# Optimization experiments

Measured on AMD Instinct MI355X. Metric: run time of the kernel, lower is better.

## Reference

```python
import jax, jax.numpy as jnp
import numpy as np

B, N, E, H = 16, 1024, 1024, 16
D = E // H  # head size = 64

def setup_inputs() -> dict:
    key = jax.random.key(0)
    ks = jax.random.split(key, 5)
    s = 1.0 / np.sqrt(E)
    return {
        "x": jax.random.normal(ks[0], (B, N, E), dtype=jnp.float32),
        "W_qkv": jax.random.normal(ks[1], (E, 3 * E), dtype=jnp.float32) * s,
        "b_qkv": jnp.zeros((3 * E,), dtype=jnp.float32),
        "W_proj": jax.random.normal(ks[2], (E, E), dtype=jnp.float32) * s,
        "b_proj": jnp.zeros((E,), dtype=jnp.float32),
    }

def reference(x, W_qkv, b_qkv, W_proj, b_proj):
    # qkv projection: [B,N,3E]
    qkv = x @ W_qkv + b_qkv
    q, k, v = jnp.split(qkv, 3, axis=-1)
    # b n (h d) -> b h n d
    def split_heads(t):
        return t.reshape(B, N, H, D).transpose(0, 2, 1, 3)
    q, k, v = split_heads(q), split_heads(k), split_heads(v)
    scale = D ** -0.5
    attn = jnp.einsum('bhnd,bhmd->bhnm', q, k) * scale  # [B,H,N,N]
    attn = jax.nn.softmax(attn, axis=-1)
    # dropout p=0 -> identity
    o = jnp.einsum('bhnm,bhmd->bhnd', attn, v)  # [B,H,N,D]
    o = o.transpose(0, 2, 1, 3).reshape(B, N, E)  # b h n d -> b n (h d)
    return o @ W_proj + b_proj
```

## Files before the change

kernel.cpp:

```cpp
#include <hip/hip_runtime.h>
#include <hip/hip_bf16.h>
#include <math.h>

#define BB 16
#define NN 1024
#define EE 1024
#define HH 16
#define DD 64
#define THREE_E 3072
#define M_TOTAL (BB * NN)

typedef __attribute__((ext_vector_type(8))) short bf16x8;
typedef __attribute__((ext_vector_type(4))) short bf16x4;
typedef __attribute__((ext_vector_type(4))) float floatx4;

#define SCALE_Q 0.18033688011112042f

static __device__ __forceinline__ unsigned short f2bf(float f) {
    union { float f; unsigned u; } x; x.f = f;
    unsigned r = x.u + 0x7fffu + ((x.u >> 16) & 1u);
    return (unsigned short)(r >> 16);
}

static __device__ __forceinline__ bf16x8 pack8v(floatx4 a, floatx4 b) {
    union { bf16x8 v; unsigned u[4]; } r;
    __hip_bfloat162 t;
    t = __float22bfloat162_rn(make_float2(a[0], a[1])); r.u[0] = *(unsigned*)&t;
    t = __float22bfloat162_rn(make_float2(a[2], a[3])); r.u[1] = *(unsigned*)&t;
    t = __float22bfloat162_rn(make_float2(b[0], b[1])); r.u[2] = *(unsigned*)&t;
    t = __float22bfloat162_rn(make_float2(b[2], b[3])); r.u[3] = *(unsigned*)&t;
    return r.v;
}
static __device__ __forceinline__ bf16x8 pack8f(float4 a, float4 b) {
    union { bf16x8 v; unsigned u[4]; } r;
    __hip_bfloat162 t;
    t = __float22bfloat162_rn(make_float2(a.x, a.y)); r.u[0] = *(unsigned*)&t;
    t = __float22bfloat162_rn(make_float2(a.z, a.w)); r.u[1] = *(unsigned*)&t;
    t = __float22bfloat162_rn(make_float2(b.x, b.y)); r.u[2] = *(unsigned*)&t;
    t = __float22bfloat162_rn(make_float2(b.z, b.w)); r.u[3] = *(unsigned*)&t;
    return r.v;
}

#define ASYNC16(gp, lp)                                                \
    __builtin_amdgcn_global_load_lds(                                  \
        (const __attribute__((address_space(1))) void*)(gp),           \
        (__attribute__((address_space(3))) void*)(lp), 16, 0, 0)

#define DRAIN_VMEM() __asm__ __volatile__("s_waitcnt vmcnt(0)" ::: "memory")

__global__ __launch_bounds__(256) void convert_x(
    const float* __restrict__ x, unsigned short* __restrict__ xb)
{
    int i = blockIdx.x * 256 + threadIdx.x;
    const float4* xp = (const float4*)x;
    float4 a = xp[i * 2], b = xp[i * 2 + 1];
    *(bf16x8*)&xb[i * 8] = pack8f(a, b);
}

__global__ __launch_bounds__(256) void wtrans(
    const float* __restrict__ w, unsigned short* __restrict__ wt, int R, int C)
{
    __shared__ float tile[32][33];
    const int t = threadIdx.x;
    const int lr = t >> 5, lc = t & 31;
    const int r0 = blockIdx.y * 32, c0 = blockIdx.x * 32;
    #pragma unroll
    for (int p = 0; p < 4; ++p)
        tile[lr + p * 8][lc] = w[(size_t)(r0 + lr + p * 8) * C + c0 + lc];
    __syncthreads();
    #pragma unroll
    for (int p = 0; p < 4; ++p) {
        int oc = lr + p * 8;
        float v = tile[lc][oc];
        wt[(size_t)(c0 + oc) * R + r0 + lc] = f2bf(v);
    }
}

__global__ __launch_bounds__(256) void gemm_qkv_mfma(
    const unsigned short* __restrict__ xb,
    const unsigned short* __restrict__ wt,
    const float* __restrict__ bias,
    unsigned short* __restrict__ Qo, unsigned short* __restrict__ Ko,
    unsigned short* __restrict__ Vo)
{
    __shared__ __align__(16) unsigned short As[128 * 32];
    __shared__ __align__(16) unsigned short Bs[128 * 32];

    const int t = threadIdx.x;
    const int w = t >> 6, lane = t & 63;
    const int quad = lane >> 4, l15 = lane & 15;
    const int wm = w >> 1, wn = w & 1;
    const int m0 = blockIdx.y * 128;
    const int n0 = blockIdx.x * 128;
    const int srow = lane >> 2;
    const int scw = (((lane & 3) ^ ((srow ^ (srow >> 2)) & 3))) * 8;
    const int rsw = ((quad ^ ((l15 ^ (l15 >> 2)) & 3))) * 8;

    floatx4 acc[4][4];
    #pragma unroll
    for (int i = 0; i < 4; ++i)
        #pragma unroll
        for (int j = 0; j < 4; ++j) acc[i][j] = (floatx4){0.f, 0.f, 0.f, 0.f};

    for (int kk = 0; kk < EE; kk += 32) {
        #pragma unroll
        for (int r = 0; r < 2; ++r) {
            int c = w * 2 + r;
            ASYNC16(&xb[(size_t)(m0 + c * 16 + srow) * EE + kk + scw],
                    &As[c * 512]);
            ASYNC16(&wt[(size_t)(n0 + c * 16 + srow) * EE + kk + scw],
                    &Bs[c * 512]);
        }
        DRAIN_VMEM();
        __syncthreads();

        bf16x8 af[4], bf[4];
        #pragma unroll
        for (int i = 0; i < 4; ++i) {
            af[i] = *(const bf16x8*)&As[(wm * 64 + i * 16 + l15) * 32 + rsw];
            bf[i] = *(const bf16x8*)&Bs[(wn * 64 + i * 16 + l15) * 32 + rsw];
        }
        #pragma unroll
        for (int i = 0; i < 4; ++i)
            #pragma unroll
            for (int j = 0; j < 4; ++j)
                acc[i][j] = __builtin_amdgcn_mfma_f32_16x16x32_bf16(
                    af[i], bf[j], acc[i][j], 0, 0, 0);
        __syncthreads();
    }

    const int mb = m0 + wm * 64;
    const int nb = n0 + wn * 64;
    #pragma unroll
    for (int i = 0; i < 4; ++i) {
        #pragma unroll
        for (int j = 0; j < 4; ++j) {
            int nc = nb + j * 16;
            int which = nc >> 10;
            int e0 = nc & 1023;
            int h  = e0 >> 6;
            int d0 = e0 & 63;
            float bv = bias[nc + l15];
            #pragma unroll
            for (int r = 0; r < 4; ++r) {
                int m = mb + i * 16 + quad * 4 + r;
                int b = m >> 10, n = m & 1023;
                size_t off = ((size_t)(b * HH + h) * NN + n) * DD + d0 + l15;
                float v = acc[i][j][r] + bv;
                if (which == 0)      Qo[off] = f2bf(v * SCALE_Q);
                else if (which == 1) Ko[off] = f2bf(v);
                else                 Vo[off] = f2bf(v);
            }
        }
    }
}

__global__ __launch_bounds__(256) void vtrans(
    const unsigned short* __restrict__ V, unsigned short* __restrict__ Vt)
{
    __shared__ __align__(16) unsigned short tile[64][72];
    const int t  = threadIdx.x;
    const int bh = blockIdx.x;
    const int n0 = blockIdx.y * 64;
    const int r  = t >> 2, c = t & 3;

    const unsigned short* src = &V[((size_t)bh * NN + n0 + r) * DD + c * 16];
    bf16x8 v0 = *(const bf16x8*)&src[0];
    bf16x8 v1 = *(const bf16x8*)&src[8];
    #pragma unroll
    for (int k = 0; k < 8; ++k) tile[c * 16 + k][r]     = v0[k];
    #pragma unroll
    for (int k = 0; k < 8; ++k) tile[c * 16 + 8 + k][r] = v1[k];
    __syncthreads();

    unsigned short* dst = &Vt[((size_t)bh * DD + r) * NN + n0 + c * 16];
    *(bf16x8*)&dst[0] = *(const bf16x8*)&tile[r][c * 16];
    *(bf16x8*)&dst[8] = *(const bf16x8*)&tile[r][c * 16 + 8];
}

__global__ __launch_bounds__(256) void attn_mfma(
    const unsigned short* __restrict__ Q,
    const unsigned short* __restrict__ K,
    const unsigned short* __restrict__ Vt,
    unsigned short* __restrict__ O)
{
    __shared__ __align__(16) unsigned short Ks[64 * 64];
    __shared__ __align__(16) unsigned short Vs[64 * 64];

    const int t    = threadIdx.x;
    const int w    = t >> 6;
    const int quad = (t >> 4) & 3;
    const int l15  = t & 15;
    const int i    = blockIdx.x;
    const int bh   = ((i >> 6) << 3) | (i & 7);
    const int qt   = (i >> 3) & 7;

    const unsigned short* Qg = Q  + (size_t)bh * NN * DD;
    const unsigned short* Kg = K  + (size_t)bh * NN * DD;
    const unsigned short* Vg = Vt + (size_t)bh * DD * NN;

    const int q0 = qt * 128 + w * 32;

    bf16x8 qf[2][2];
    #pragma unroll
    for (int a = 0; a < 2; ++a) {
        qf[a][0] = *(const bf16x8*)&Qg[(size_t)(q0 + a * 16 + l15) * DD + quad * 8];
        qf[a][1] = *(const bf16x8*)&Qg[(size_t)(q0 + a * 16 + l15) * DD + 32 + quad * 8];
    }

    floatx4 oa[2][4];
    #pragma unroll
    for (int a = 0; a < 2; ++a)
        #pragma unroll
        for (int jd = 0; jd < 4; ++jd) oa[a][jd] = (floatx4){0.f, 0.f, 0.f, 0.f};
    float lsum[2] = {0.f, 0.f};

    const int srow = t >> 2;
    const int sc   = t & 3;
    const int swz  = srow & 7;
    const int cbase = ((quad ^ (l15 & 7)) << 3);

    bf16x8 kr0, kr1, vr0, vr1;
    {
        const unsigned short* kg = &Kg[(size_t)srow * DD + sc * 16];
        kr0 = *(const bf16x8*)&kg[0];
        kr1 = *(const bf16x8*)&kg[8];
        const unsigned short* vg = &Vg[(size_t)srow * NN + sc * 16];
        vr0 = *(const bf16x8*)&vg[0];
        vr1 = *(const bf16x8*)&vg[8];
    }

    for (int kt = 0; kt < 16; ++kt) {
        __syncthreads();
        *(bf16x8*)&Ks[srow * 64 + (((2 * sc + 0) ^ swz) << 3)] = kr0;
        *(bf16x8*)&Ks[srow * 64 + (((2 * sc + 1) ^ swz) << 3)] = kr1;
        {
            bf16x4 h[4];
            h[0] = (bf16x4){vr0[0], vr0[1], vr0[2], vr0[3]};
            h[1] = (bf16x4){vr0[4], vr0[5], vr0[6], vr0[7]};
            h[2] = (bf16x4){vr1[0], vr1[1], vr1[2], vr1[3]};
            h[3] = (bf16x4){vr1[4], vr1[5], vr1[6], vr1[7]};
            #pragma unroll
            for (int q = 0; q < 4; ++q) {
                int col = ((((sc >> 1) * 4 + q) ^ swz) << 3) + ((sc & 1) << 2);
                *(bf16x4*)&Vs[srow * 64 + col] = h[q];
            }
        }
        __syncthreads();

        if (kt < 15) {
            const unsigned short* kg =
                &Kg[(size_t)((kt + 1) * 64 + srow) * DD + sc * 16];
            kr0 = *(const bf16x8*)&kg[0];
            kr1 = *(const bf16x8*)&kg[8];
            const unsigned short* vg =
                &Vg[(size_t)srow * NN + (kt + 1) * 64 + sc * 16];
            vr0 = *(const bf16x8*)&vg[0];
            vr1 = *(const bf16x8*)&vg[8];
        }

        floatx4 sa[2][4];
        #pragma unroll
        for (int a = 0; a < 2; ++a)
            #pragma unroll
            for (int tt = 0; tt < 4; ++tt) sa[a][tt] = (floatx4){0.f, 0.f, 0.f, 0.f};
        #pragma unroll
        for (int tt = 0; tt < 4; ++tt) {
            const unsigned short* kb = &Ks[(tt * 16 + l15) * 64];
            bf16x8 kf0 = *(const bf16x8*)&kb[cbase];
            bf16x8 kf1 = *(const bf16x8*)&kb[cbase ^ 32];
            #pragma unroll
            for (int a = 0; a < 2; ++a) {
                sa[a][tt] = __builtin_amdgcn_mfma_f32_16x16x32_bf16(
                    kf0, qf[a][0], sa[a][tt], 0, 0, 0);
                sa[a][tt] = __builtin_amdgcn_mfma_f32_16x16x32_bf16(
                    kf1, qf[a][1], sa[a][tt], 0, 0, 0);
            }
        }

        bf16x8 pf[2][2];
        #pragma unroll
        for (int a = 0; a < 2; ++a) {
            floatx4 pe[4];
            #pragma unroll
            for (int tt = 0; tt < 4; ++tt) {
                #pragma unroll
                for (int r = 0; r < 4; ++r) {
                    float p = exp2f(sa[a][tt][r]);
                    pe[tt][r] = p;
                    lsum[a] += p;
                }
            }
            pf[a][0] = pack8v(pe[0], pe[1]);
            pf[a][1] = pack8v(pe[2], pe[3]);
        }

        #pragma unroll
        for (int jd = 0; jd < 4; ++jd) {
            const unsigned short* vb = &Vs[(jd * 16 + l15) * 64];
            bf16x8 vf0 = *(const bf16x8*)&vb[cbase];
            bf16x8 vf1 = *(const bf16x8*)&vb[cbase ^ 32];
            #pragma unroll
            for (int a = 0; a < 2; ++a) {
                oa[a][jd] = __builtin_amdgcn_mfma_f32_16x16x32_bf16(
                    vf0, pf[a][0], oa[a][jd], 0, 0, 0);
                oa[a][jd] = __builtin_amdgcn_mfma_f32_16x16x32_bf16(
                    vf1, pf[a][1], oa[a][jd], 0, 0, 0);
            }
        }
    }

    #pragma unroll
    for (int a = 0; a < 2; ++a) {
        lsum[a] += __shfl_xor(lsum[a], 16, 64);
        lsum[a] += __shfl_xor(lsum[a], 32, 64);
    }

    const int b = bh >> 4, h = bh & 15;
    #pragma unroll
    for (int a = 0; a < 2; ++a) {
        float inv = 1.f / lsum[a];
        int n = q0 + a * 16 + l15;
        size_t base = (size_t)(b * NN + n) * EE + h * DD;
        #pragma unroll
        for (int jd = 0; jd < 4; ++jd) {
            bf16x4 v;
            v[0] = (short)f2bf(oa[a][jd][0] * inv);
            v[1] = (short)f2bf(oa[a][jd][1] * inv);
            v[2] = (short)f2bf(oa[a][jd][2] * inv);
            v[3] = (short)f2bf(oa[a][jd][3] * inv);
            *(bf16x4*)&O[base + jd * 16 + quad * 4] = v;
        }
    }
}

__global__ __launch_bounds__(256) void gemm_proj_mfma(
    const unsigned short* __restrict__ Ob,
    const unsigned short* __restrict__ Bp,
    const float* __restrict__ bias, float* __restrict__ out)
{
    __shared__ __align__(16) unsigned short As[128 * 32];
    __shared__ __align__(16) unsigned short Bs[128 * 32];

    const int t = threadIdx.x;
    const int w = t >> 6, lane = t & 63;
    const int quad = lane >> 4, l15 = lane & 15;
    const int wm = w >> 1, wn = w & 1;
    const int m0 = blockIdx.y * 128;
    const int n0 = blockIdx.x * 128;
    const int srow = lane >> 2;
    const int scw = (((lane & 3) ^ ((srow ^ (srow >> 2)) & 3))) * 8;
    const int rsw = ((quad ^ ((l15 ^ (l15 >> 2)) & 3))) * 8;

    floatx4 acc[4][4];
    #pragma unroll
    for (int i = 0; i < 4; ++i)
        #pragma unroll
        for (int j = 0; j < 4; ++j) acc[i][j] = (floatx4){0.f, 0.f, 0.f, 0.f};

    for (int kk = 0; kk < EE; kk += 32) {
        #pragma unroll
        for (int r = 0; r < 2; ++r) {
            int c = w * 2 + r;
            ASYNC16(&Ob[(size_t)(m0 + c * 16 + srow) * EE + kk + scw],
                    &As[c * 512]);
            ASYNC16(&Bp[(size_t)(n0 + c * 16 + srow) * EE + kk + scw],
                    &Bs[c * 512]);
        }
        DRAIN_VMEM();
        __syncthreads();

        bf16x8 af[4], bf[4];
        #pragma unroll
        for (int i = 0; i < 4; ++i) {
            af[i] = *(const bf16x8*)&As[(wm * 64 + i * 16 + l15) * 32 + rsw];
            bf[i] = *(const bf16x8*)&Bs[(wn * 64 + i * 16 + l15) * 32 + rsw];
        }
        #pragma unroll
        for (int i = 0; i < 4; ++i)
            #pragma unroll
            for (int j = 0; j < 4; ++j)
                acc[i][j] = __builtin_amdgcn_mfma_f32_16x16x32_bf16(
                    af[i], bf[j], acc[i][j], 0, 0, 0);
        __syncthreads();
    }

    const int mb = m0 + wm * 64;
    const int nb = n0 + wn * 64;
    #pragma unroll
    for (int i = 0; i < 4; ++i) {
        #pragma unroll
        for (int j = 0; j < 4; ++j) {
            float bv = bias[nb + j * 16 + l15];
            #pragma unroll
            for (int r = 0; r < 4; ++r) {
                int mrow = mb + i * 16 + quad * 4 + r;
                out[(size_t)mrow * EE + nb + j * 16 + l15] = acc[i][j][r] + bv;
            }
        }
    }
}

extern "C" void kernel_launch(void* const* d_in, const int* in_sizes, int n_in,
                              void* d_out, int out_size, void* d_ws, size_t ws_size,
                              hipStream_t stream) {
    const float* x     = (const float*)d_in[0];
    const float* Wqkv  = (const float*)d_in[1];
    const float* bqkv  = (const float*)d_in[2];
    const float* Wproj = (const float*)d_in[3];
    const float* bproj = (const float*)d_in[4];
    float* out = (float*)d_out;

    const size_t BHND = (size_t)BB * HH * NN * DD;
    unsigned short* Q   = (unsigned short*)d_ws;
    unsigned short* K   = Q   + BHND;
    unsigned short* Vn  = K   + BHND;
    unsigned short* Vt  = Vn  + BHND;
    unsigned short* Ob  = Vt  + BHND;
    unsigned short* xb  = Ob  + BHND;
    unsigned short* Wqt = xb  + BHND;
    unsigned short* Wpt = Wqt + (size_t)THREE_E * EE;

    dim3 blk(256);
    convert_x<<<dim3(M_TOTAL * EE / (256 * 8)), blk, 0, stream>>>(x, xb);
    wtrans<<<dim3(THREE_E / 32, EE / 32), blk, 0, stream>>>(Wqkv, Wqt, EE, THREE_E);
    wtrans<<<dim3(EE / 32, EE / 32), blk, 0, stream>>>(Wproj, Wpt, EE, EE);

    gemm_qkv_mfma<<<dim3(THREE_E / 128, M_TOTAL / 128), blk, 0, stream>>>(
        xb, Wqt, bqkv, Q, K, Vn);
    vtrans<<<dim3(BB * HH, NN / 64), blk, 0, stream>>>(Vn, Vt);
    attn_mfma<<<dim3(BB * HH * NN / 128), blk, 0, stream>>>(Q, K, Vt, Ob);
    gemm_proj_mfma<<<dim3(EE / 128, M_TOTAL / 128), blk, 0, stream>>>(
        Ob, Wpt, bproj, out);
}
```

Before: 447.2 us.

## Pipeline QKV and projection GEMMs with 256x256 tiles and 4-stage async LDS

Both GEMMs move from 128x128 tiles with 256 threads and a full vmem drain every k-step to 256x256 tiles with 512 threads and a 4-slot LDS ring. Global-to-LDS loads are issued three steps ahead and split between the two MFMA halves, with partial vmcnt waits, raw barriers and s_setprio around the MFMA blocks. The block index is remapped across 8 groups, likely to spread tiles over XCDs for better cache locality. The change targets exposed load latency and low arithmetic intensity, at the cost of more registers (8x4 accumulators) and 128KB of LDS per block, which may limit occupancy.

```diff
diff --git a/kernel.cpp b/kernel.cpp
--- a/kernel.cpp
+++ b/kernel.cpp
@@ -46,8 +46,6 @@
         (const __attribute__((address_space(1))) void*)(gp),           \
         (__attribute__((address_space(3))) void*)(lp), 16, 0, 0)
 
-#define DRAIN_VMEM() __asm__ __volatile__("s_waitcnt vmcnt(0)" ::: "memory")
-
 __global__ __launch_bounds__(256) void convert_x(
     const float* __restrict__ x, unsigned short* __restrict__ xb)
 {
@@ -76,66 +74,107 @@
     }
 }
 
-__global__ __launch_bounds__(256) void gemm_qkv_mfma(
+#define GNT 32
+
+__global__ __launch_bounds__(512, 2) void gemm_qkv_mfma(
     const unsigned short* __restrict__ xb,
     const unsigned short* __restrict__ wt,
     const float* __restrict__ bias,
     unsigned short* __restrict__ Qo, unsigned short* __restrict__ Ko,
     unsigned short* __restrict__ Vo)
 {
-    __shared__ __align__(16) unsigned short As[128 * 32];
-    __shared__ __align__(16) unsigned short Bs[128 * 32];
+    __shared__ __align__(16) unsigned short As[4][256 * 32];
+    __shared__ __align__(16) unsigned short Bs[4][256 * 32];
 
     const int t = threadIdx.x;
     const int w = t >> 6, lane = t & 63;
     const int quad = lane >> 4, l15 = lane & 15;
-    const int wm = w >> 1, wn = w & 1;
-    const int m0 = blockIdx.y * 128;
-    const int n0 = blockIdx.x * 128;
+    const int wm = w >> 2, wn = w & 3;
+
+    const int id  = blockIdx.x;
+    const int sid = (id & 7) * ((int)gridDim.x >> 3) + (id >> 3);
+    const int m0 = (sid / 12) * 256;
+    const int n0 = (sid % 12) * 256;
+
     const int srow = lane >> 2;
     const int scw = (((lane & 3) ^ ((srow ^ (srow >> 2)) & 3))) * 8;
     const int rsw = ((quad ^ ((l15 ^ (l15 >> 2)) & 3))) * 8;
 
-    floatx4 acc[4][4];
-    #pragma unroll
-    for (int i = 0; i < 4; ++i)
+    const unsigned short* aG = &xb[(size_t)(m0 + w * 16 + srow) * EE + scw];
+    const unsigned short* bG = &wt[(size_t)(n0 + w * 16 + srow) * EE + scw];
+    const int ldsW = (w * 16) * 32;
+
+#define STG_A(c) do { const int sl_ = (c) & 3;                          \
+    ASYNC16(aG + (c) * 32,            &As[sl_][ldsW]);                  \
+    ASYNC16(aG + (c) * 32 + 128 * EE, &As[sl_][ldsW + 128 * 32]); } while (0)
+#define STG_B(c) do { const int sl_ = (c) & 3;                          \
+    ASYNC16(bG + (c) * 32,            &Bs[sl_][ldsW]);                  \
+    ASYNC16(bG + (c) * 32 + 128 * EE, &Bs[sl_][ldsW + 128 * 32]); } while (0)
+
+    floatx4 acc[8][4];
+    #pragma unroll
+    for (int i = 0; i < 8; ++i)
         #pragma unroll
         for (int j = 0; j < 4; ++j) acc[i][j] = (floatx4){0.f, 0.f, 0.f, 0.f};
 
-    for (int kk = 0; kk < EE; kk += 32) {
-        #pragma unroll
-        for (int r = 0; r < 2; ++r) {
-            int c = w * 2 + r;
-            ASYNC16(&xb[(size_t)(m0 + c * 16 + srow) * EE + kk + scw],
-                    &As[c * 512]);
-            ASYNC16(&wt[(size_t)(n0 + c * 16 + srow) * EE + kk + scw],
-                    &Bs[c * 512]);
-        }
-        DRAIN_VMEM();
-        __syncthreads();
-
-        bf16x8 af[4], bf[4];
-        #pragma unroll
-        for (int i = 0; i < 4; ++i) {
-            af[i] = *(const bf16x8*)&As[(wm * 64 + i * 16 + l15) * 32 + rsw];
-            bf[i] = *(const bf16x8*)&Bs[(wn * 64 + i * 16 + l15) * 32 + rsw];
-        }
+    STG_A(0); STG_B(0); STG_A(1); STG_B(1); STG_A(2); STG_B(2);
+    __asm__ __volatile__("s_waitcnt vmcnt(8)" ::: "memory");
+    __builtin_amdgcn_s_barrier();
+
+    #pragma unroll 1
+    for (int c = 0; c < GNT; ++c) {
+        const unsigned short* Asl = As[c & 3];
+        const unsigned short* Bsl = Bs[c & 3];
+        bf16x8 bfr[4], afr[4];
+
+        #pragma unroll
+        for (int j = 0; j < 4; ++j)
+            bfr[j] = *(const bf16x8*)&Bsl[(wn * 64 + j * 16 + l15) * 32 + rsw];
+        #pragma unroll
+        for (int i = 0; i < 4; ++i)
+            afr[i] = *(const bf16x8*)&Asl[(wm * 128 + i * 16 + l15) * 32 + rsw];
+        if (c + 3 < GNT) STG_A(c + 3);
+        __builtin_amdgcn_s_barrier();
+        __asm__ __volatile__("s_waitcnt lgkmcnt(0)" ::: "memory");
+        __builtin_amdgcn_s_setprio(1);
         #pragma unroll
         for (int i = 0; i < 4; ++i)
             #pragma unroll
             for (int j = 0; j < 4; ++j)
                 acc[i][j] = __builtin_amdgcn_mfma_f32_16x16x32_bf16(
-                    af[i], bf[j], acc[i][j], 0, 0, 0);
-        __syncthreads();
-    }
-
-    const int mb = m0 + wm * 64;
-    const int nb = n0 + wn * 64;
-    #pragma unroll
-    for (int i = 0; i < 4; ++i) {
+                    afr[i], bfr[j], acc[i][j], 0, 0, 0);
+        __builtin_amdgcn_s_setprio(0);
+        __builtin_amdgcn_s_barrier();
+
+        #pragma unroll
+        for (int i = 0; i < 4; ++i)
+            afr[i] = *(const bf16x8*)&Asl[(wm * 128 + 64 + i * 16 + l15) * 32 + rsw];
+        if (c + 3 < GNT) STG_B(c + 3);
+        __builtin_amdgcn_s_barrier();
+        __asm__ __volatile__("s_waitcnt lgkmcnt(0)" ::: "memory");
+        __builtin_amdgcn_s_setprio(1);
+        #pragma unroll
+        for (int i = 0; i < 4; ++i)
+            #pragma unroll
+            for (int j = 0; j < 4; ++j)
+                acc[4 + i][j] = __builtin_amdgcn_mfma_f32_16x16x32_bf16(
+                    afr[i], bfr[j], acc[4 + i][j], 0, 0, 0);
+        __builtin_amdgcn_s_setprio(0);
+        if (c < GNT - 3)       { __asm__ __volatile__("s_waitcnt vmcnt(8)" ::: "memory"); }
+        else if (c == GNT - 3) { __asm__ __volatile__("s_waitcnt vmcnt(4)" ::: "memory"); }
+        else if (c == GNT - 2) { __asm__ __volatile__("s_waitcnt vmcnt(0)" ::: "memory"); }
+        __builtin_amdgcn_s_barrier();
+    }
+#undef STG_A
+#undef STG_B
+
+    const int mb = m0 + wm * 128;
+    const int nbase = n0 + wn * 64;
+    #pragma unroll
+    for (int i = 0; i < 8; ++i) {
         #pragma unroll
         for (int j = 0; j < 4; ++j) {
-            int nc = nb + j * 16;
+            int nc = nbase + j * 16;
             int which = nc >> 10;
             int e0 = nc & 1023;
             int h  = e0 >> 6;
@@ -334,68 +373,107 @@
     }
 }
 
-__global__ __launch_bounds__(256) void gemm_proj_mfma(
+__global__ __launch_bounds__(512, 2) void gemm_proj_mfma(
     const unsigned short* __restrict__ Ob,
     const unsigned short* __restrict__ Bp,
     const float* __restrict__ bias, float* __restrict__ out)
 {
-    __shared__ __align__(16) unsigned short As[128 * 32];
-    __shared__ __align__(16) unsigned short Bs[128 * 32];
+    __shared__ __align__(16) unsigned short As[4][256 * 32];
+    __shared__ __align__(16) unsigned short Bs[4][256 * 32];
 
     const int t = threadIdx.x;
     const int w = t >> 6, lane = t & 63;
     const int quad = lane >> 4, l15 = lane & 15;
-    const int wm = w >> 1, wn = w & 1;
-    const int m0 = blockIdx.y * 128;
-    const int n0 = blockIdx.x * 128;
+    const int wm = w >> 2, wn = w & 3;
+
+    const int id  = blockIdx.x;
+    const int sid = (id & 7) * ((int)gridDim.x >> 3) + (id >> 3);
+    const int m0 = (sid / 4) * 256;
+    const int n0 = (sid % 4) * 256;
+
     const int srow = lane >> 2;
     const int scw = (((lane & 3) ^ ((srow ^ (srow >> 2)) & 3))) * 8;
     const int rsw = ((quad ^ ((l15 ^ (l15 >> 2)) & 3))) * 8;
 
-    floatx4 acc[4][4];
-    #pragma unroll
-    for (int i = 0; i < 4; ++i)
+    const unsigned short* aG = &Ob[(size_t)(m0 + w * 16 + srow) * EE + scw];
+    const unsigned short* bG = &Bp[(size_t)(n0 + w * 16 + srow) * EE + scw];
+    const int ldsW = (w * 16) * 32;
+
+#define STG_A(c) do { const int sl_ = (c) & 3;                          \
+    ASYNC16(aG + (c) * 32,            &As[sl_][ldsW]);                  \
+    ASYNC16(aG + (c) * 32 + 128 * EE, &As[sl_][ldsW + 128 * 32]); } while (0)
+#define STG_B(c) do { const int sl_ = (c) & 3;                          \
+    ASYNC16(bG + (c) * 32,            &Bs[sl_][ldsW]);                  \
+    ASYNC16(bG + (c) * 32 + 128 * EE, &Bs[sl_][ldsW + 128 * 32]); } while (0)
+
+    floatx4 acc[8][4];
+    #pragma unroll
+    for (int i = 0; i < 8; ++i)
         #pragma unroll
         for (int j = 0; j < 4; ++j) acc[i][j] = (floatx4){0.f, 0.f, 0.f, 0.f};
 
-    for (int kk = 0; kk < EE; kk += 32) {
-        #pragma unroll
-        for (int r = 0; r < 2; ++r) {
-            int c = w * 2 + r;
-            ASYNC16(&Ob[(size_t)(m0 + c * 16 + srow) * EE + kk + scw],
-                    &As[c * 512]);
-            ASYNC16(&Bp[(size_t)(n0 + c * 16 + srow) * EE + kk + scw],
-                    &Bs[c * 512]);
-        }
-        DRAIN_VMEM();
-        __syncthreads();
-
-        bf16x8 af[4], bf[4];
-        #pragma unroll
-        for (int i = 0; i < 4; ++i) {
-            af[i] = *(const bf16x8*)&As[(wm * 64 + i * 16 + l15) * 32 + rsw];
-            bf[i] = *(const bf16x8*)&Bs[(wn * 64 + i * 16 + l15) * 32 + rsw];
-        }
+    STG_A(0); STG_B(0); STG_A(1); STG_B(1); STG_A(2); STG_B(2);
+    __asm__ __volatile__("s_waitcnt vmcnt(8)" ::: "memory");
+    __builtin_amdgcn_s_barrier();
+
+    #pragma unroll 1
+    for (int c = 0; c < GNT; ++c) {
+        const unsigned short* Asl = As[c & 3];
+        const unsigned short* Bsl = Bs[c & 3];
+        bf16x8 bfr[4], afr[4];
+
+        #pragma unroll
+        for (int j = 0; j < 4; ++j)
+            bfr[j] = *(const bf16x8*)&Bsl[(wn * 64 + j * 16 + l15) * 32 + rsw];
+        #pragma unroll
+        for (int i = 0; i < 4; ++i)
+            afr[i] = *(const bf16x8*)&Asl[(wm * 128 + i * 16 + l15) * 32 + rsw];
+        if (c + 3 < GNT) STG_A(c + 3);
+        __builtin_amdgcn_s_barrier();
+        __asm__ __volatile__("s_waitcnt lgkmcnt(0)" ::: "memory");
+        __builtin_amdgcn_s_setprio(1);
         #pragma unroll
         for (int i = 0; i < 4; ++i)
             #pragma unroll
             for (int j = 0; j < 4; ++j)
                 acc[i][j] = __builtin_amdgcn_mfma_f32_16x16x32_bf16(
-                    af[i], bf[j], acc[i][j], 0, 0, 0);
-        __syncthreads();
-    }
-
-    const int mb = m0 + wm * 64;
-    const int nb = n0 + wn * 64;
-    #pragma unroll
-    for (int i = 0; i < 4; ++i) {
+                    afr[i], bfr[j], acc[i][j], 0, 0, 0);
+        __builtin_amdgcn_s_setprio(0);
+        __builtin_amdgcn_s_barrier();
+
+        #pragma unroll
+        for (int i = 0; i < 4; ++i)
+            afr[i] = *(const bf16x8*)&Asl[(wm * 128 + 64 + i * 16 + l15) * 32 + rsw];
+        if (c + 3 < GNT) STG_B(c + 3);
+        __builtin_amdgcn_s_barrier();
+        __asm__ __volatile__("s_waitcnt lgkmcnt(0)" ::: "memory");
+        __builtin_amdgcn_s_setprio(1);
+        #pragma unroll
+        for (int i = 0; i < 4; ++i)
+            #pragma unroll
+            for (int j = 0; j < 4; ++j)
+                acc[4 + i][j] = __builtin_amdgcn_mfma_f32_16x16x32_bf16(
+                    afr[i], bfr[j], acc[4 + i][j], 0, 0, 0);
+        __builtin_amdgcn_s_setprio(0);
+        if (c < GNT - 3)       { __asm__ __volatile__("s_waitcnt vmcnt(8)" ::: "memory"); }
+        else if (c == GNT - 3) { __asm__ __volatile__("s_waitcnt vmcnt(4)" ::: "memory"); }
+        else if (c == GNT - 2) { __asm__ __volatile__("s_waitcnt vmcnt(0)" ::: "memory"); }
+        __builtin_amdgcn_s_barrier();
+    }
+#undef STG_A
+#undef STG_B
+
+    const int mb = m0 + wm * 128;
+    const int nbase = n0 + wn * 64;
+    #pragma unroll
+    for (int i = 0; i < 8; ++i) {
         #pragma unroll
         for (int j = 0; j < 4; ++j) {
-            float bv = bias[nb + j * 16 + l15];
+            float bv = bias[nbase + j * 16 + l15];
             #pragma unroll
             for (int r = 0; r < 4; ++r) {
                 int mrow = mb + i * 16 + quad * 4 + r;
-                out[(size_t)mrow * EE + nb + j * 16 + l15] = acc[i][j][r] + bv;
+                out[(size_t)mrow * EE + nbase + j * 16 + l15] = acc[i][j][r] + bv;
             }
         }
     }
@@ -426,10 +504,10 @@
     wtrans<<<dim3(THREE_E / 32, EE / 32), blk, 0, stream>>>(Wqkv, Wqt, EE, THREE_E);
     wtrans<<<dim3(EE / 32, EE / 32), blk, 0, stream>>>(Wproj, Wpt, EE, EE);
 
-    gemm_qkv_mfma<<<dim3(THREE_E / 128, M_TOTAL / 128), blk, 0, stream>>>(
+    gemm_qkv_mfma<<<dim3((M_TOTAL / 256) * (THREE_E / 256)), dim3(512), 0, stream>>>(
         xb, Wqt, bqkv, Q, K, Vn);
     vtrans<<<dim3(BB * HH, NN / 64), blk, 0, stream>>>(Vn, Vt);
     attn_mfma<<<dim3(BB * HH * NN / 128), blk, 0, stream>>>(Q, K, Vt, Ob);
-    gemm_proj_mfma<<<dim3(EE / 128, M_TOTAL / 128), blk, 0, stream>>>(
+    gemm_proj_mfma<<<dim3((M_TOTAL / 256) * (EE / 256)), dim3(512), 0, stream>>>(
         Ob, Wpt, bproj, out);
 }
```

Measured after the change: 426.8 us. -4.6%, faster.
